# Kernel tuning notes

Measured on AMD Instinct MI355X. Metric: run time of the kernel, lower is better.

## Reference

```python
import jax, jax.numpy as jnp
import numpy as np

B, Q, L, D = 4, 600, 2048, 256
H, HD, DFF, KD = 8, 32, 2048, 32  # heads, head_dim, ffn dim, gasa kernel dim
SCALE = HD ** -0.5


def setup_inputs() -> dict:
    key = jax.random.key(0)
    ks = jax.random.split(key, 24)
    w = lambda k, shape, s=0.02: (jax.random.normal(k, shape, jnp.float32) * s)
    inp = {
        "queries": jax.random.normal(ks[0], (B, Q, D), jnp.float32),
        "memory": jax.random.normal(ks[1], (B, L, D), jnp.float32),
        "memory_pos": jax.random.normal(ks[2], (B, L, 3), jnp.float32),
        "query_pos": jax.random.normal(ks[3], (B, Q, 3), jnp.float32),
        # self-attention (nn.MultiheadAttention packed in_proj)
        "sa_in_w": w(ks[4], (3 * D, D)), "sa_in_b": jnp.zeros((3 * D,), jnp.float32),
        "sa_out_w": w(ks[5], (D, D)), "sa_out_b": jnp.zeros((D,), jnp.float32),
        "norm1_g": jnp.ones((D,), jnp.float32), "norm1_b": jnp.zeros((D,), jnp.float32),
        # cross-attention projections
        "q_w": w(ks[6], (D, D)), "q_b": jnp.zeros((D,), jnp.float32),
        "k_w": w(ks[7], (D, D)), "k_b": jnp.zeros((D,), jnp.float32),
        "v_w": w(ks[8], (D, D)), "v_b": jnp.zeros((D,), jnp.float32),
        "o_w": w(ks[9], (D, D)), "o_b": jnp.zeros((D,), jnp.float32),
        "norm2_g": jnp.ones((D,), jnp.float32), "norm2_b": jnp.zeros((D,), jnp.float32),
        # GASA geometric-bias kernel: beta, MLP 1->KD->1
        "beta": jnp.asarray(1.0, jnp.float32),
        "dk_w1": w(ks[10], (KD, 1), 0.1), "dk_b1": jnp.zeros((KD,), jnp.float32),
        "dk_w2": w(ks[11], (1, KD), 0.1), "dk_b2": jnp.full((1,), -1.0, jnp.float32),
        # FFN
        "ffn_w1": w(ks[12], (DFF, D)), "ffn_b1": jnp.zeros((DFF,), jnp.float32),
        "ffn_w2": w(ks[13], (D, DFF)), "ffn_b2": jnp.zeros((D,), jnp.float32),
        "norm3_g": jnp.ones((D,), jnp.float32), "norm3_b": jnp.zeros((D,), jnp.float32),
    }
    return inp


def _ln(x, g, b, eps=1e-5):
    m = jnp.mean(x, -1, keepdims=True)
    v = jnp.mean((x - m) ** 2, -1, keepdims=True)
    return (x - m) * jax.lax.rsqrt(v + eps) * g + b


def _heads(x, wt, b):  # x:[B,N,D] -> [B,H,N,HD]
    y = x @ wt.T + b
    return y.reshape(x.shape[0], x.shape[1], H, HD).transpose(0, 2, 1, 3)


def reference(queries, memory, memory_pos, query_pos,
              sa_in_w, sa_in_b, sa_out_w, sa_out_b, norm1_g, norm1_b,
              q_w, q_b, k_w, k_b, v_w, v_b, o_w, o_b, norm2_g, norm2_b,
              beta, dk_w1, dk_b1, dk_w2, dk_b2,
              ffn_w1, ffn_b1, ffn_w2, ffn_b2, norm3_g, norm3_b):
    # ---- self-attention (post-norm, no query_pe) ----
    wq, wk, wv = jnp.split(sa_in_w, 3, axis=0)
    bq, bk, bv = jnp.split(sa_in_b, 3)
    qh = _heads(queries, wq, bq)
    kh = _heads(queries, wk, bk)
    vh = _heads(queries, wv, bv)
    a = jax.nn.softmax(jnp.einsum('bhqd,bhkd->bhqk', qh, kh) * SCALE, axis=-1)
    sa = jnp.einsum('bhqk,bhkd->bhqd', a, vh).transpose(0, 2, 1, 3).reshape(B, Q, D)
    sa = sa @ sa_out_w.T + sa_out_b
    x = _ln(queries + sa, norm1_g, norm1_b)

    # ---- GASA cross-attention ----
    Qh = _heads(x, q_w, q_b)          # [B,H,Q,HD]
    Kh = _heads(memory, k_w, k_b)     # [B,H,L,HD]
    Vh = _heads(memory, v_w, v_b)     # [B,H,L,HD]
    # cdist + learned kernel MLP, clamp to [-10, 0] (suppress-only)
    d2 = jnp.sum((query_pos[:, :, None, :] - memory_pos[:, None, :, :]) ** 2, -1)
    dist = jnp.sqrt(jnp.maximum(d2, 0.0))                     # [B,Q,L]
    hid = jax.nn.relu(dist[..., None] * dk_w1[:, 0] + dk_b1)  # [B,Q,L,KD]
    bias = (hid @ dk_w2[0]) + dk_b2[0]                        # [B,Q,L]
    bias = jnp.clip(bias, -10.0, 0.0)
    scores = jnp.einsum('bhqd,bhkd->bhqk', Qh, Kh) * SCALE + beta * bias[:, None]
    attn = jax.nn.softmax(scores, axis=-1)
    ca = jnp.einsum('bhqk,bhkd->bhqd', attn, Vh).transpose(0, 2, 1, 3).reshape(B, Q, D)
    ca = ca @ o_w.T + o_b
    x = _ln(x + ca, norm2_g, norm2_b)

    # ---- FFN (post-norm) ----
    f = jax.nn.relu(x @ ffn_w1.T + ffn_b1) @ ffn_w2.T + ffn_b2
    return _ln(x + f, norm3_g, norm3_b)
```

## Files before the change

kernel.cpp:

```cpp
#include <hip/hip_runtime.h>
#include <hip/hip_bf16.h>

typedef __hip_bfloat16 bf16;
typedef __attribute__((ext_vector_type(8))) short  short8;
typedef __attribute__((ext_vector_type(4))) short  short4v;
typedef __attribute__((ext_vector_type(4))) float  f32x4;

#define B_ 4
#define Q_ 600
#define L_ 2048
#define D_ 256
#define H_ 8
#define HD_ 32
#define DFF_ 2048
#define KD_ 32
#define SCALE_ 0.17677669529663687f
#define L2E_   1.4426950408889634f
#define SL2E_  (SCALE_ * L2E_)

__device__ __forceinline__ float fexp2(float x) { return __builtin_amdgcn_exp2f(x); }

__device__ __forceinline__ bool detect_f32_inline(const unsigned short* __restrict__ q)
{
    const int lane = threadIdx.x & 63;
    float m = 0.f;
    #pragma unroll
    for (int i = 0; i < 4; i++) {
        unsigned short u = q[lane + i * 64];
        float f = __uint_as_float(((unsigned)(u & 0x7FFF)) << 16);
        if (f != f) f = 1e30f;
        m = fmaxf(m, f);
    }
    #pragma unroll
    for (int o = 32; o > 0; o >>= 1) m = fmaxf(m, __shfl_xor(m, o));
    return m > 100.f;
}

template<int MODE>
__device__ __forceinline__ float ldx(const void* p, size_t i, bool f32)
{
    if (MODE == 0) return __bfloat162float(((const bf16*)p)[i]);
    if (MODE == 1) return ((const float*)p)[i];
    return f32 ? ((const float*)p)[i] : __bfloat162float(((const bf16*)p)[i]);
}
__device__ __forceinline__ short8 ld8_f32(const float* p)
{
    const float4 a = *(const float4*)p;
    const float4 b = *(const float4*)(p + 4);
    union { short8 s; bf16 h[8]; } u;
    u.h[0] = __float2bfloat16(a.x); u.h[1] = __float2bfloat16(a.y);
    u.h[2] = __float2bfloat16(a.z); u.h[3] = __float2bfloat16(a.w);
    u.h[4] = __float2bfloat16(b.x); u.h[5] = __float2bfloat16(b.y);
    u.h[6] = __float2bfloat16(b.z); u.h[7] = __float2bfloat16(b.w);
    return u.s;
}
template<int MODE>
__device__ __forceinline__ short8 ld8x(const void* p, size_t i, bool f32)
{
    if (MODE == 0) return *(const short8*)((const bf16*)p + i);
    if (MODE == 1) return ld8_f32((const float*)p + i);
    return f32 ? ld8_f32((const float*)p + i) : *(const short8*)((const bf16*)p + i);
}

template<int NSEG>
__device__ __forceinline__ short8 ld8_comb(const bf16* __restrict__ pO,
                                           const float* __restrict__ pml,
                                           int row, int col)
{
    const unsigned b = (unsigned)row / 600u;
    const unsigned q = (unsigned)row - b * 600u;
    const int h = col >> 5, dd = col & 31;
    const unsigned rp = b * 4800u + (unsigned)h * 600u + q;
    float W = 0.f;
    float acc[8] = {0.f,0.f,0.f,0.f,0.f,0.f,0.f,0.f};
    #pragma unroll
    for (int s = 0; s < NSEG; s++) {
        const size_t rr = (size_t)s * 19200u + rp;
        const float l = pml[rr * 2 + 1];
        W += l;
        const short8 o = *(const short8*)(pO + rr * 32 + dd);
        #pragma unroll
        for (int j = 0; j < 8; j++)
            acc[j] += l * __bfloat162float(((const bf16*)&o)[j]);
    }
    const float inv = 1.f / W;
    union { short8 s; bf16 h8[8]; } u;
    #pragma unroll
    for (int j = 0; j < 8; j++) u.h8[j] = __float2bfloat16(acc[j] * inv);
    return u.s;
}

template<int AM, int NSEG>
__device__ __forceinline__ void gemm_core(const void* __restrict__ A,
    const void* __restrict__ W, int M, int K, int kbeg, int kend,
    int bm, int bn, bool f32, bf16* As, bf16* Bs, f32x4 (&acc)[2][2],
    const float* __restrict__ pml)
{
    const int tid = threadIdx.x;
    const int w = tid >> 6, lane = tid & 63;
    const int quad = lane >> 4, l16 = lane & 15;
    const int wm = (w & 1) << 5, wn = (w >> 1) << 5;
    const int srow = tid >> 2, scol = (tid & 3) << 3;
    const int gma = (bm + srow < M) ? bm + srow : M - 1;

    short8 pa, pb;
    if constexpr (AM == 3) pa = ld8_comb<NSEG>((const bf16*)A, pml, gma, kbeg + scol);
    else                   pa = ld8x<AM>(A, (size_t)gma * K + kbeg + scol, f32);
    pb = ld8x<2>(W, (size_t)(bn + srow) * K + kbeg + scol, f32);

    for (int k0 = kbeg; k0 < kend; k0 += 32) {
        *(short8*)&As[srow * 40 + scol] = pa;
        *(short8*)&Bs[srow * 40 + scol] = pb;
        __syncthreads();
        if (k0 + 32 < kend) {
            if constexpr (AM == 3) pa = ld8_comb<NSEG>((const bf16*)A, pml, gma, k0 + 32 + scol);
            else                   pa = ld8x<AM>(A, (size_t)gma * K + k0 + 32 + scol, f32);
            pb = ld8x<2>(W, (size_t)(bn + srow) * K + k0 + 32 + scol, f32);
        }
        short8 af[2], bfr[2];
        #pragma unroll
        for (int t = 0; t < 2; t++) {
            af[t]  = *(const short8*)&As[(wm + t * 16 + l16) * 40 + quad * 8];
            bfr[t] = *(const short8*)&Bs[(wn + t * 16 + l16) * 40 + quad * 8];
        }
        #pragma unroll
        for (int mt = 0; mt < 2; mt++)
            #pragma unroll
            for (int nt = 0; nt < 2; nt++)
                acc[mt][nt] = __builtin_amdgcn_mfma_f32_16x16x32_bf16(
                    af[mt], bfr[nt], acc[mt][nt], 0, 0, 0);
        __syncthreads();
    }
}

template<int RM, int CM, bool RELU>
__device__ __forceinline__ void gemm_epi(const f32x4 (&acc)[2][2],
    const void* __restrict__ bias, const void* __restrict__ R,
    void* __restrict__ C, int M, int N, int bm, int bn, bool f32)
{
    const int tid = threadIdx.x;
    const int w = tid >> 6, lane = tid & 63;
    const int quad = lane >> 4, l16 = lane & 15;
    const int wm = (w & 1) << 5, wn = (w >> 1) << 5;
    #pragma unroll
    for (int mt = 0; mt < 2; mt++) {
        #pragma unroll
        for (int r = 0; r < 4; r++) {
            const int row = bm + wm + mt * 16 + quad * 4 + r;
            if (row >= M) continue;
            #pragma unroll
            for (int nt = 0; nt < 2; nt++) {
                const int col = bn + wn + nt * 16 + l16;
                float v = acc[mt][nt][r] + ldx<2>(bias, col, f32);
                if (RM >= 0) v += ldx<(RM < 0 ? 0 : RM)>(R, (size_t)row * N + col, f32);
                if (RELU) v = fmaxf(v, 0.f);
                if (CM == 0) ((bf16*)C)[(size_t)row * N + col] = __float2bfloat16(v);
                else         ((float*)C)[(size_t)row * N + col] = v;
            }
        }
    }
}

template<int AM, int RM, int CM, bool RELU, int SPLIT, int NSEG>
__global__ __launch_bounds__(256)
void gemm_mfma(const void* __restrict__ A, const void* __restrict__ W,
               const void* __restrict__ bias, const void* __restrict__ R,
               void* __restrict__ C, int M, int N, int K,
               const unsigned short* __restrict__ qdet,
               const float* __restrict__ pml)
{
    const bool f32 = detect_f32_inline(qdet);
    __shared__ alignas(16) bf16 As[64 * 40];
    __shared__ alignas(16) bf16 Bs[64 * 40];
    const int bm = blockIdx.y << 6, bn = blockIdx.x << 6;
    const int KS = K / SPLIT, z = (SPLIT > 1) ? blockIdx.z : 0;

    f32x4 acc[2][2] = {{{0.f,0.f,0.f,0.f},{0.f,0.f,0.f,0.f}},
                       {{0.f,0.f,0.f,0.f},{0.f,0.f,0.f,0.f}}};
    gemm_core<AM, NSEG>(A, W, M, K, z * KS, z * KS + KS, bm, bn, f32, As, Bs, acc, pml);

    if (SPLIT > 1) {
        const int tid = threadIdx.x;
        const int w = tid >> 6, lane = tid & 63;
        const int quad = lane >> 4, l16 = lane & 15;
        const int wm = (w & 1) << 5, wn = (w >> 1) << 5;
        #pragma unroll
        for (int mt = 0; mt < 2; mt++)
            #pragma unroll
            for (int r = 0; r < 4; r++) {
                const int row = bm + wm + mt * 16 + quad * 4 + r;
                if (row >= M) continue;
                #pragma unroll
                for (int nt = 0; nt < 2; nt++) {
                    const int col = bn + wn + nt * 16 + l16;
                    ((float*)C)[((size_t)z * M + row) * N + col] = acc[mt][nt][r];
                }
            }
    } else {
        gemm_epi<RM, CM, RELU>(acc, bias, R, C, M, N, bm, bn, f32);
    }
}

__global__ __launch_bounds__(256)
void proj3(const void* __restrict__ queries,
           const void* __restrict__ sa_in_w, const void* __restrict__ sa_in_b,
           bf16* __restrict__ qkv,
           const void* __restrict__ memory,
           const void* __restrict__ kw, const void* __restrict__ kb,
           const void* __restrict__ vw, const void* __restrict__ vb,
           bf16* __restrict__ kf, bf16* __restrict__ vf)
{
    const bool f32 = detect_f32_inline((const unsigned short*)queries);
    __shared__ alignas(16) bf16 As[64 * 40];
    __shared__ alignas(16) bf16 Bs[64 * 40];
    const int bid = blockIdx.x;

    const void *A, *W, *bsp;
    void* C;
    int M, N, bm, bn;
    if (bid < 456) {
        A = queries; W = sa_in_w; bsp = sa_in_b; C = qkv;
        M = 2400; N = 768;
        bm = (bid / 12) << 6; bn = (bid % 12) << 6;
    } else {
        const int id = bid - 456;
        const int sel = (id & 7) >> 2;
        A = memory; W = sel ? vw : kw; bsp = sel ? vb : kb;
        C = sel ? (void*)vf : (void*)kf;
        M = 8192; N = 256;
        bm = (id >> 3) << 6; bn = (id & 3) << 6;
    }

    f32x4 acc[2][2] = {{{0.f,0.f,0.f,0.f},{0.f,0.f,0.f,0.f}},
                       {{0.f,0.f,0.f,0.f},{0.f,0.f,0.f,0.f}}};
    gemm_core<2, 1>(A, W, M, 256, 0, 256, bm, bn, f32, As, Bs, acc, nullptr);
    gemm_epi<-1, 0, false>(acc, bsp, nullptr, C, M, N, bm, bn, f32);
}

__global__ __launch_bounds__(256)
void bias_pre(const void* __restrict__ qp, const void* __restrict__ mp,
              const void* __restrict__ w1, const void* __restrict__ b1,
              const void* __restrict__ w2, const void* __restrict__ b2,
              const void* __restrict__ betap, bf16* __restrict__ out,
              const unsigned short* __restrict__ qdet)
{
    const bool f32 = detect_f32_inline(qdet);
    __shared__ float sw1[KD_], sb1[KD_], sw2[KD_], scst[2];
    const int tid = threadIdx.x;
    if (tid < KD_) {
        sw1[tid] = ldx<2>(w1, tid, f32);
        sb1[tid] = ldx<2>(b1, tid, f32);
        sw2[tid] = ldx<2>(w2, tid, f32);
    }
    if (tid == 0) { scst[0] = ldx<2>(b2, 0, f32); scst[1] = L2E_ * ldx<2>(betap, 0, f32); }
    __syncthreads();
    const int idx = blockIdx.x * 256 + tid;
    const int q8 = idx % 75;
    const int t2 = idx / 75;
    const int l = t2 % L_, b = t2 / L_;
    const int q0 = q8 * 8;
    const float mx = ldx<2>(mp, (size_t)(b * L_ + l) * 3 + 0, f32);
    const float my = ldx<2>(mp, (size_t)(b * L_ + l) * 3 + 1, f32);
    const float mz = ldx<2>(mp, (size_t)(b * L_ + l) * 3 + 2, f32);

    float dist[8];
    #pragma unroll
    for (int j = 0; j < 8; j++) {
        const int q = q0 + j;
        float dx = ldx<2>(qp, (size_t)(b * Q_ + q) * 3 + 0, f32) - mx;
        float dy = ldx<2>(qp, (size_t)(b * Q_ + q) * 3 + 1, f32) - my;
        float dz = ldx<2>(qp, (size_t)(b * Q_ + q) * 3 + 2, f32) - mz;
        dist[j] = sqrtf(dx * dx + dy * dy + dz * dz);
    }
    float acc[8];
    const float a0 = scst[0];
    #pragma unroll
    for (int j = 0; j < 8; j++) acc[j] = a0;
    #pragma unroll
    for (int k = 0; k < KD_; k++) {
        const float c1 = sw1[k], c0 = sb1[k], c2 = sw2[k];
        #pragma unroll
        for (int j = 0; j < 8; j++)
            acc[j] += fmaxf(dist[j] * c1 + c0, 0.f) * c2;
    }
    union { short8 s; bf16 h[8]; } res;
    const float sc = scst[1];
    #pragma unroll
    for (int j = 0; j < 8; j++) {
        float a = fminf(fmaxf(acc[j], -10.f), 0.f);
        res.h[j] = __float2bfloat16(sc * a);
    }
    *(short8*)(out + ((size_t)(b * L_) + l) * Q_ + q0) = res.s;
}

template<bool HASBIAS, int NSEG>
__global__ __launch_bounds__(256)
void flash_attn(const bf16* __restrict__ Qm, int qs,
                const bf16* __restrict__ Km, int ks,
                const bf16* __restrict__ Vm, int vs,
                const bf16* __restrict__ biasT,
                bf16* __restrict__ pO, float* __restrict__ pml,
                int NQ, int LK)
{
    __shared__ alignas(16) bf16 Ksh[64 * 40];
    __shared__ alignas(16) bf16 Vt[48 * 72];
    __shared__ alignas(16) bf16 Psh[64 * 72];
    __shared__ alignas(16) bf16 Bsh[HASBIAS ? 64 * 72 : 8];

    const int tid = threadIdx.x;
    const int w = tid >> 6, lane = tid & 63;
    const int quad = lane >> 4, l16 = lane & 15;

    const int id = blockIdx.x;
    const int g  = ((id >> 6) << 3) + (id & 7);
    const int h  = (id >> 3) & 7;
    const int qt = g % 10;
    const int zz = g / 10;
    const int b = zz & 3, seg = zz >> 2;
    const int q0 = qt * 64;
    const int segLen = LK / NSEG;
    const int lbeg = seg * segLen, lend = lbeg + segLen;

    for (int i = tid; i < 16 * 72; i += 256) {
        int rr = 32 + i / 72, cc = i % 72;
        Vt[rr * 72 + cc] = __float2bfloat16(rr == 32 ? 1.f : 0.f);
    }

    int qrow = q0 + w * 16 + l16; if (qrow > NQ - 1) qrow = NQ - 1;
    const short8 aq = *(const short8*)(Qm + (size_t)(b * NQ + qrow) * qs + h * HD_ + quad * 8);

    f32x4 O0 = {0.f,0.f,0.f,0.f}, O1 = {0.f,0.f,0.f,0.f}, O2 = {0.f,0.f,0.f,0.f};

    const int srow = tid >> 2, sc4 = tid & 3;
    const int nch = (segLen + 63) >> 6;

    const int ll0 = tid >> 3, ll1 = ll0 + 32, qc = tid & 7;
    int qr = q0 + qc * 8; if (qr > NQ - 8) qr = NQ - 8;

    int lg0 = lbeg + srow; if (lg0 > LK - 1) lg0 = LK - 1;
    short8 k8 = *(const short8*)(Km + (size_t)(b * LK + lg0) * ks + h * HD_ + sc4 * 8);
    short8 v8 = *(const short8*)(Vm + (size_t)(b * LK + lg0) * vs + h * HD_ + sc4 * 8);
    short8 bb0, bb1;
    if (HASBIAS) {
        bb0 = *(const short8*)(biasT + ((size_t)(b * LK) + lbeg + ll0) * Q_ + qr);
        bb1 = *(const short8*)(biasT + ((size_t)(b * LK) + lbeg + ll1) * Q_ + qr);
    }

    for (int ch = 0; ch < nch; ch++) {
        const int l0 = lbeg + (ch << 6);
        *(short8*)&Ksh[srow * 40 + sc4 * 8] = k8;
        {
            const int swc = srow ^ (sc4 * 16);
            #pragma unroll
            for (int j = 0; j < 8; j++)
                Vt[(sc4 * 8 + j) * 72 + swc] = ((const bf16*)&v8)[j];
        }
        if (HASBIAS) {
            *(short8*)&Bsh[ll0 * 72 + qc * 8] = bb0;
            *(short8*)&Bsh[ll1 * 72 + qc * 8] = bb1;
        }
        __syncthreads();

        if (ch + 1 < nch) {
            const int l0n = l0 + 64;
            int lg = l0n + srow; if (lg > LK - 1) lg = LK - 1;
            k8 = *(const short8*)(Km + (size_t)(b * LK + lg) * ks + h * HD_ + sc4 * 8);
            v8 = *(const short8*)(Vm + (size_t)(b * LK + lg) * vs + h * HD_ + sc4 * 8);
            if (HASBIAS) {
                bb0 = *(const short8*)(biasT + ((size_t)(b * LK) + l0n + ll0) * Q_ + qr);
                bb1 = *(const short8*)(biasT + ((size_t)(b * LK) + l0n + ll1) * Q_ + qr);
            }
        }

        f32x4 sv[4];
        #pragma unroll
        for (int jt = 0; jt < 4; jt++) {
            short8 kb = *(const short8*)&Ksh[(jt * 16 + l16) * 40 + quad * 8];
            sv[jt] = __builtin_amdgcn_mfma_f32_16x16x32_bf16(aq, kb, (f32x4){0.f,0.f,0.f,0.f}, 0, 0, 0);
        }
        if (l0 + 64 <= lend) {
            #pragma unroll
            for (int jt = 0; jt < 4; jt++) {
                if (HASBIAS) {
                    short4v bb = *(const short4v*)&Bsh[(jt * 16 + l16) * 72 + w * 16 + quad * 4];
                    #pragma unroll
                    for (int r = 0; r < 4; r++)
                        Psh[(w * 16 + quad * 4 + r) * 72 + jt * 16 + l16] =
                            __float2bfloat16(fexp2(sv[jt][r] * SL2E_ +
                                __bfloat162float(((const bf16*)&bb)[r])));
                } else {
                    #pragma unroll
                    for (int r = 0; r < 4; r++)
                        Psh[(w * 16 + quad * 4 + r) * 72 + jt * 16 + l16] =
                            __float2bfloat16(fexp2(sv[jt][r] * SL2E_));
                }
            }
        } else {
            #pragma unroll
            for (int jt = 0; jt < 4; jt++) {
                const bool valid = (l0 + jt * 16 + l16) < lend;
                #pragma unroll
                for (int r = 0; r < 4; r++)
                    Psh[(w * 16 + quad * 4 + r) * 72 + jt * 16 + l16] =
                        __float2bfloat16(valid ? fexp2(sv[jt][r] * SL2E_) : 0.f);
            }
        }
        const int sw0 = 16 * (l16 >> 3);
        const int sw1 = 16 * (2 + (l16 >> 3));
        #pragma unroll
        for (int kt = 0; kt < 2; kt++) {
            short8 ap  = *(const short8*)&Psh[(w * 16 + l16) * 72 + kt * 32 + quad * 8];
            short8 bv0 = *(const short8*)&Vt[(l16) * 72 + ((kt * 32 + quad * 8) ^ sw0)];
            short8 bv1 = *(const short8*)&Vt[(16 + l16) * 72 + ((kt * 32 + quad * 8) ^ sw1)];
            short8 bon = *(const short8*)&Vt[(32 + l16) * 72 + kt * 32 + quad * 8];
            O0 = __builtin_amdgcn_mfma_f32_16x16x32_bf16(ap, bv0, O0, 0, 0, 0);
            O1 = __builtin_amdgcn_mfma_f32_16x16x32_bf16(ap, bv1, O1, 0, 0, 0);
            O2 = __builtin_amdgcn_mfma_f32_16x16x32_bf16(ap, bon, O2, 0, 0, 0);
        }
        __syncthreads();
    }

    #pragma unroll
    for (int r = 0; r < 4; r++) {
        const int qg = q0 + w * 16 + quad * 4 + r;
        if (qg >= NQ) continue;
        const float li = __shfl(O2[r], lane & 48);
        const float inv = 1.f / li;
        const size_t rowp = (size_t)(((seg * 4 + b) * 8) + h) * NQ + qg;
        bf16* op = pO + rowp * 32;
        op[l16]      = __float2bfloat16(O0[r] * inv);
        op[16 + l16] = __float2bfloat16(O1[r] * inv);
        if (l16 == 0) pml[rowp * 2 + 1] = O2[r];
    }
}

template<int RM, int OM, int S>
__global__ __launch_bounds__(64)
void red_ln(const float* __restrict__ P, const void* __restrict__ bias,
            const void* __restrict__ R, const void* __restrict__ gg,
            const void* __restrict__ bb, void* __restrict__ Y,
            int M, const unsigned short* __restrict__ qdet)
{
    const bool f32 = detect_f32_inline(qdet);
    const int row = blockIdx.x, lane = threadIdx.x;
    const int d0 = lane * 4;
    float v[4];
    {
        float4 a = *(const float4*)(P + ((size_t)0 * M + row) * D_ + d0);
        v[0] = a.x; v[1] = a.y; v[2] = a.z; v[3] = a.w;
    }
    #pragma unroll
    for (int s = 1; s < S; s++) {
        float4 a = *(const float4*)(P + ((size_t)s * M + row) * D_ + d0);
        v[0] += a.x; v[1] += a.y; v[2] += a.z; v[3] += a.w;
    }
    #pragma unroll
    for (int j = 0; j < 4; j++)
        v[j] += ldx<2>(bias, d0 + j, f32) + ldx<RM>(R, (size_t)row * D_ + d0 + j, f32);

    float s1 = v[0] + v[1] + v[2] + v[3];
    float s2 = v[0]*v[0] + v[1]*v[1] + v[2]*v[2] + v[3]*v[3];
    #pragma unroll
    for (int o = 32; o > 0; o >>= 1) {
        s1 += __shfl_xor(s1, o);
        s2 += __shfl_xor(s2, o);
    }
    const float mean = s1 * (1.f / D_);
    const float var = s2 * (1.f / D_) - mean * mean;
    const float rinv = rsqrtf(var + 1e-5f);
    float o[4];
    #pragma unroll
    for (int j = 0; j < 4; j++)
        o[j] = (v[j] - mean) * rinv * ldx<2>(gg, d0 + j, f32) + ldx<2>(bb, d0 + j, f32);
    const size_t i = (size_t)row * D_ + d0;
    if (OM == 1 || (OM == 2 && f32)) {
        float4 t{o[0], o[1], o[2], o[3]};
        *(float4*)((float*)Y + i) = t;
    } else {
        bf16* y = (bf16*)Y + i;
        y[0] = __float2bfloat16(o[0]); y[1] = __float2bfloat16(o[1]);
        y[2] = __float2bfloat16(o[2]); y[3] = __float2bfloat16(o[3]);
    }
}

extern "C" void kernel_launch(void* const* d_in, const int* in_sizes, int n_in,
                              void* d_out, int out_size, void* d_ws, size_t ws_size,
                              hipStream_t stream)
{
    const void* queries   = d_in[0];
    const void* memory    = d_in[1];
    const void* memory_pos= d_in[2];
    const void* query_pos = d_in[3];
    const void* sa_in_w   = d_in[4];
    const void* sa_in_b   = d_in[5];
    const void* sa_out_w  = d_in[6];
    const void* sa_out_b  = d_in[7];
    const void* norm1_g   = d_in[8];
    const void* norm1_b   = d_in[9];
    const void* q_w  = d_in[10], *q_b  = d_in[11];
    const void* k_w  = d_in[12], *k_b  = d_in[13];
    const void* v_w  = d_in[14], *v_b  = d_in[15];
    const void* o_w  = d_in[16], *o_b  = d_in[17];
    const void* norm2_g = d_in[18], *norm2_b = d_in[19];
    const void* beta  = d_in[20];
    const void* dk_w1 = d_in[21], *dk_b1 = d_in[22];
    const void* dk_w2 = d_in[23], *dk_b2 = d_in[24];
    const void* ffn_w1 = d_in[25], *ffn_b1 = d_in[26];
    const void* ffn_w2 = d_in[27], *ffn_b2 = d_in[28];
    const void* norm3_g = d_in[29], *norm3_b = d_in[30];

    const unsigned short* qdet = (const unsigned short*)queries;

    char* base = (char*)d_ws;
    bf16*  kf      = (bf16*)(base + 0);
    bf16*  vf      = (bf16*)(base + 4194304);
    bf16*  biasT   = (bf16*)(base + 8388608);
    bf16*  qkv     = (bf16*)(base + 18219008);
    bf16*  selfO   = (bf16*)(base + 21905408);
    float* selfML  = (float*)(base + 24363008);
    float* P3      = (float*)(base + 24670208);
    float* x1      = (float*)(base + 18219008);
    bf16*  qproj   = (bf16*)(base + 20676608);
    bf16*  crossO  = (bf16*)(base + 21905408);
    float* crossML = (float*)(base + 26820608);
    float* P10     = (float*)(base + 0);
    float* x2      = (float*)(base + 4915200);
    bf16*  ffnh    = (bf16*)(base + 7372800);
    float* P13     = (float*)(base + 17203200);

    const dim3 blk(256);

    proj3<<<1480, blk, 0, stream>>>(
        queries, sa_in_w, sa_in_b, qkv,
        memory, k_w, k_b, v_w, v_b, kf, vf);
    bias_pre<<<2400, blk, 0, stream>>>(
        query_pos, memory_pos, dk_w1, dk_b1, dk_w2, dk_b2, beta, biasT, qdet);
    flash_attn<false, 2><<<640, blk, 0, stream>>>(
        qkv, 768, qkv + 256, 768, qkv + 512, 768, nullptr,
        selfO, selfML, 600, 600);
    gemm_mfma<3, -1, 1, false, 2, 2><<<dim3(4, 38, 2), blk, 0, stream>>>(
        selfO, sa_out_w, nullptr, nullptr, P3, 2400, 256, 256, qdet, selfML);
    red_ln<2, 1, 2><<<2400, 64, 0, stream>>>(
        P3, sa_out_b, queries, norm1_g, norm1_b, x1, 2400, qdet);
    gemm_mfma<1, -1, 0, false, 1, 1><<<dim3(4, 38), blk, 0, stream>>>(
        x1, q_w, q_b, nullptr, qproj, 2400, 256, 256, qdet, nullptr);
    flash_attn<true, 4><<<1280, blk, 0, stream>>>(
        qproj, 256, kf, 256, vf, 256, biasT,
        crossO, crossML, 600, 2048);
    gemm_mfma<3, -1, 1, false, 2, 4><<<dim3(4, 38, 2), blk, 0, stream>>>(
        crossO, o_w, nullptr, nullptr, P10, 2400, 256, 256, qdet, crossML);
    red_ln<1, 1, 2><<<2400, 64, 0, stream>>>(
        P10, o_b, x1, norm2_g, norm2_b, x2, 2400, qdet);
    gemm_mfma<1, -1, 0, true, 1, 1><<<dim3(32, 38), blk, 0, stream>>>(
        x2, ffn_w1, ffn_b1, nullptr, ffnh, 2400, 2048, 256, qdet, nullptr);
    gemm_mfma<0, -1, 1, false, 4, 1><<<dim3(4, 38, 4), blk, 0, stream>>>(
        ffnh, ffn_w2, nullptr, nullptr, P13, 2400, 256, 2048, qdet, nullptr);
    red_ln<1, 2, 4><<<2400, 64, 0, stream>>>(
        P13, ffn_b2, x2, norm3_g, norm3_b, d_out, 2400, qdet);
}
```

Baseline: 276.3 us.

## Fuse split-K reduction and LayerNorm into GEMM via last-block atomic counter

```diff
diff --git a/kernel.cpp b/kernel.cpp
--- a/kernel.cpp
+++ b/kernel.cpp
@@ -161,13 +161,16 @@
     }
 }
 
-template<int AM, int RM, int CM, bool RELU, int SPLIT, int NSEG>
+template<int AM, int RM, int CM, bool RELU, int SPLIT, int NSEG, int LNRM, int LNOM>
 __global__ __launch_bounds__(256)
 void gemm_mfma(const void* __restrict__ A, const void* __restrict__ W,
                const void* __restrict__ bias, const void* __restrict__ R,
                void* __restrict__ C, int M, int N, int K,
                const unsigned short* __restrict__ qdet,
-               const float* __restrict__ pml)
+               const float* __restrict__ pml,
+               const void* __restrict__ lnR, const void* __restrict__ gg,
+               const void* __restrict__ bb, void* __restrict__ Y,
+               int* __restrict__ ctr)
 {
     const bool f32 = detect_f32_inline(qdet);
     __shared__ alignas(16) bf16 As[64 * 40];
@@ -179,8 +182,8 @@
                        {{0.f,0.f,0.f,0.f},{0.f,0.f,0.f,0.f}}};
     gemm_core<AM, NSEG>(A, W, M, K, z * KS, z * KS + KS, bm, bn, f32, As, Bs, acc, pml);
 
+    const int tid = threadIdx.x;
     if (SPLIT > 1) {
-        const int tid = threadIdx.x;
         const int w = tid >> 6, lane = tid & 63;
         const int quad = lane >> 4, l16 = lane & 15;
         const int wm = (w & 1) << 5, wn = (w >> 1) << 5;
@@ -196,6 +199,68 @@
                     ((float*)C)[((size_t)z * M + row) * N + col] = acc[mt][nt][r];
                 }
             }
+        if constexpr (LNRM >= 0) {
+            __shared__ int lastf;
+            __threadfence();
+            __syncthreads();
+            if (tid == 0)
+                lastf = (atomicAdd(&ctr[blockIdx.y], 1) ==
+                         (int)(gridDim.x * gridDim.z) - 1);
+            __syncthreads();
+            if (lastf) {
+                __threadfence();
+                const float* P = (const float*)C;
+                const int wv = tid >> 6, ln = tid & 63;
+                const int d0 = ln * 4;
+                float gb[4], gvv[4], bvv[4];
+                #pragma unroll
+                for (int j = 0; j < 4; j++) {
+                    gb[j]  = ldx<2>(bias, d0 + j, f32);
+                    gvv[j] = ldx<2>(gg, d0 + j, f32);
+                    bvv[j] = ldx<2>(bb, d0 + j, f32);
+                }
+                for (int it = 0; it < 16; it++) {
+                    const int row = bm + it * 4 + wv;
+                    if (row >= M) continue;
+                    float v[4];
+                    {
+                        float4 a = *(const float4*)(P + (size_t)row * 256 + d0);
+                        v[0] = a.x; v[1] = a.y; v[2] = a.z; v[3] = a.w;
+                    }
+                    #pragma unroll
+                    for (int s = 1; s < SPLIT; s++) {
+                        float4 a = *(const float4*)(P + ((size_t)s * M + row) * 256 + d0);
+                        v[0] += a.x; v[1] += a.y; v[2] += a.z; v[3] += a.w;
+                    }
+                    #pragma unroll
+                    for (int j = 0; j < 4; j++)
+                        v[j] += gb[j] + ldx<(LNRM < 0 ? 0 : LNRM)>(lnR, (size_t)row * 256 + d0 + j, f32);
+                    float s1 = v[0] + v[1] + v[2] + v[3];
+                    float s2 = v[0]*v[0] + v[1]*v[1] + v[2]*v[2] + v[3]*v[3];
+                    #pragma unroll
+                    for (int o = 32; o > 0; o >>= 1) {
+                        s1 += __shfl_xor(s1, o);
+                        s2 += __shfl_xor(s2, o);
+                    }
+                    const float mean = s1 * (1.f / 256.f);
+                    const float var  = s2 * (1.f / 256.f) - mean * mean;
+                    const float rinv = rsqrtf(var + 1e-5f);
+                    float o4[4];
+                    #pragma unroll
+                    for (int j = 0; j < 4; j++)
+                        o4[j] = (v[j] - mean) * rinv * gvv[j] + bvv[j];
+                    const size_t i = (size_t)row * 256 + d0;
+                    if (LNOM == 1 || (LNOM == 2 && f32)) {
+                        float4 t{o4[0], o4[1], o4[2], o4[3]};
+                        *(float4*)((float*)Y + i) = t;
+                    } else {
+                        bf16* y = (bf16*)Y + i;
+                        y[0] = __float2bfloat16(o4[0]); y[1] = __float2bfloat16(o4[1]);
+                        y[2] = __float2bfloat16(o4[2]); y[3] = __float2bfloat16(o4[3]);
+                    }
+                }
+            }
+        }
     } else {
         gemm_epi<RM, CM, RELU>(acc, bias, R, C, M, N, bm, bn, f32);
     }
@@ -208,12 +273,14 @@
            const void* __restrict__ memory,
            const void* __restrict__ kw, const void* __restrict__ kb,
            const void* __restrict__ vw, const void* __restrict__ vb,
-           bf16* __restrict__ kf, bf16* __restrict__ vf)
+           bf16* __restrict__ kf, bf16* __restrict__ vf,
+           int* __restrict__ ctrbase)
 {
     const bool f32 = detect_f32_inline((const unsigned short*)queries);
     __shared__ alignas(16) bf16 As[64 * 40];
     __shared__ alignas(16) bf16 Bs[64 * 40];
     const int bid = blockIdx.x;
+    if (bid == 0 && threadIdx.x < 128) ctrbase[threadIdx.x] = 0;
 
     const void *A, *W, *bsp;
     void* C;
@@ -434,55 +501,6 @@
     }
 }
 
-template<int RM, int OM, int S>
-__global__ __launch_bounds__(64)
-void red_ln(const float* __restrict__ P, const void* __restrict__ bias,
-            const void* __restrict__ R, const void* __restrict__ gg,
-            const void* __restrict__ bb, void* __restrict__ Y,
-            int M, const unsigned short* __restrict__ qdet)
-{
-    const bool f32 = detect_f32_inline(qdet);
-    const int row = blockIdx.x, lane = threadIdx.x;
-    const int d0 = lane * 4;
-    float v[4];
-    {
-        float4 a = *(const float4*)(P + ((size_t)0 * M + row) * D_ + d0);
-        v[0] = a.x; v[1] = a.y; v[2] = a.z; v[3] = a.w;
-    }
-    #pragma unroll
-    for (int s = 1; s < S; s++) {
-        float4 a = *(const float4*)(P + ((size_t)s * M + row) * D_ + d0);
-        v[0] += a.x; v[1] += a.y; v[2] += a.z; v[3] += a.w;
-    }
-    #pragma unroll
-    for (int j = 0; j < 4; j++)
-        v[j] += ldx<2>(bias, d0 + j, f32) + ldx<RM>(R, (size_t)row * D_ + d0 + j, f32);
-
-    float s1 = v[0] + v[1] + v[2] + v[3];
-    float s2 = v[0]*v[0] + v[1]*v[1] + v[2]*v[2] + v[3]*v[3];
-    #pragma unroll
-    for (int o = 32; o > 0; o >>= 1) {
-        s1 += __shfl_xor(s1, o);
-        s2 += __shfl_xor(s2, o);
-    }
-    const float mean = s1 * (1.f / D_);
-    const float var = s2 * (1.f / D_) - mean * mean;
-    const float rinv = rsqrtf(var + 1e-5f);
-    float o[4];
-    #pragma unroll
-    for (int j = 0; j < 4; j++)
-        o[j] = (v[j] - mean) * rinv * ldx<2>(gg, d0 + j, f32) + ldx<2>(bb, d0 + j, f32);
-    const size_t i = (size_t)row * D_ + d0;
-    if (OM == 1 || (OM == 2 && f32)) {
-        float4 t{o[0], o[1], o[2], o[3]};
-        *(float4*)((float*)Y + i) = t;
-    } else {
-        bf16* y = (bf16*)Y + i;
-        y[0] = __float2bfloat16(o[0]); y[1] = __float2bfloat16(o[1]);
-        y[2] = __float2bfloat16(o[2]); y[3] = __float2bfloat16(o[3]);
-    }
-}
-
 extern "C" void kernel_launch(void* const* d_in, const int* in_sizes, int n_in,
                               void* d_out, int out_size, void* d_ws, size_t ws_size,
                               hipStream_t stream)
@@ -527,34 +545,35 @@
     float* x2      = (float*)(base + 4915200);
     bf16*  ffnh    = (bf16*)(base + 7372800);
     float* P13     = (float*)(base + 17203200);
+    int*   ctrs    = (int*)(base + 29585408);
+    int*   ctr0 = ctrs, *ctr1 = ctrs + 38, *ctr2 = ctrs + 76;
 
     const dim3 blk(256);
 
     proj3<<<1480, blk, 0, stream>>>(
         queries, sa_in_w, sa_in_b, qkv,
-        memory, k_w, k_b, v_w, v_b, kf, vf);
+        memory, k_w, k_b, v_w, v_b, kf, vf, ctrs);
     bias_pre<<<2400, blk, 0, stream>>>(
         query_pos, memory_pos, dk_w1, dk_b1, dk_w2, dk_b2, beta, biasT, qdet);
     flash_attn<false, 2><<<640, blk, 0, stream>>>(
         qkv, 768, qkv + 256, 768, qkv + 512, 768, nullptr,
         selfO, selfML, 600, 600);
-    gemm_mfma<3, -1, 1, false, 2, 2><<<dim3(4, 38, 2), blk, 0, stream>>>(
-        selfO, sa_out_w, nullptr, nullptr, P3, 2400, 256, 256, qdet, selfML);
-    red_ln<2, 1, 2><<<2400, 64, 0, stream>>>(
-        P3, sa_out_b, queries, norm1_g, norm1_b, x1, 2400, qdet);
-    gemm_mfma<1, -1, 0, false, 1, 1><<<dim3(4, 38), blk, 0, stream>>>(
-        x1, q_w, q_b, nullptr, qproj, 2400, 256, 256, qdet, nullptr);
+    gemm_mfma<3, -1, 1, false, 2, 2, 2, 1><<<dim3(4, 38, 2), blk, 0, stream>>>(
+        selfO, sa_out_w, sa_out_b, nullptr, P3, 2400, 256, 256, qdet, selfML,
+        queries, norm1_g, norm1_b, x1, ctr0);
+    gemm_mfma<1, -1, 0, false, 1, 1, -9, 0><<<dim3(4, 38), blk, 0, stream>>>(
+        x1, q_w, q_b, nullptr, qproj, 2400, 256, 256, qdet, nullptr,
+        nullptr, nullptr, nullptr, nullptr, nullptr);
     flash_attn<true, 4><<<1280, blk, 0, stream>>>(
         qproj, 256, kf, 256, vf, 256, biasT,
         crossO, crossML, 600, 2048);
-    gemm_mfma<3, -1, 1, false, 2, 4><<<dim3(4, 38, 2), blk, 0, stream>>>(
-        crossO, o_w, nullptr, nullptr, P10, 2400, 256, 256, qdet, crossML);
-    red_ln<1, 1, 2><<<2400, 64, 0, stream>>>(
-        P10, o_b, x1, norm2_g, norm2_b, x2, 2400, qdet);
-    gemm_mfma<1, -1, 0, true, 1, 1><<<dim3(32, 38), blk, 0, stream>>>(
-        x2, ffn_w1, ffn_b1, nullptr, ffnh, 2400, 2048, 256, qdet, nullptr);
-    gemm_mfma<0, -1, 1, false, 4, 1><<<dim3(4, 38, 4), blk, 0, stream>>>(
-        ffnh, ffn_w2, nullptr, nullptr, P13, 2400, 256, 2048, qdet, nullptr);
-    red_ln<1, 2, 4><<<2400, 64, 0, stream>>>(
-        P13, ffn_b2, x2, norm3_g, norm3_b, d_out, 2400, qdet);
-}
+    gemm_mfma<3, -1, 1, false, 2, 4, 1, 1><<<dim3(4, 38, 2), blk, 0, stream>>>(
+        crossO, o_w, o_b, nullptr, P10, 2400, 256, 256, qdet, crossML,
+        x1, norm2_g, norm2_b, x2, ctr1);
+    gemm_mfma<1, -1, 0, true, 1, 1, -9, 0><<<dim3(32, 38), blk, 0, stream>>>(
+        x2, ffn_w1, ffn_b1, nullptr, ffnh, 2400, 2048, 256, qdet, nullptr,
+        nullptr, nullptr, nullptr, nullptr, nullptr);
+    gemm_mfma<0, -1, 1, false, 4, 1, 1, 2><<<dim3(4, 38, 4), blk, 0, stream>>>(
+        ffnh, ffn_w2, ffn_b2, nullptr, P13, 2400, 256, 2048, qdet, nullptr,
+        x2, norm3_g, norm3_b, d_out, ctr2);
+}
```

Result: slower. 471.9 us (+70.8%).
